# Optimization experiments

Measured on AMD Instinct MI355X. Metric: run time of the kernel, lower is better.

Reference implementation:

```python
import jax, jax.numpy as jnp
import numpy as np

B, H, W, C, NH, K = 4, 56, 56, 128, 4, 7


def setup_inputs() -> dict:
    key = jax.random.key(0)
    ks = jax.random.split(key, 6)
    x = jax.random.normal(ks[0], (B, H, W, C), dtype=jnp.float32)
    w_qkv = jax.random.normal(ks[1], (C, 3 * C), dtype=jnp.float32) * 0.02
    b_qkv = jnp.zeros((3 * C,), dtype=jnp.float32)
    rpb = jax.random.normal(ks[2], (NH, 2 * K - 1, 2 * K - 1), dtype=jnp.float32) * 0.02
    w_proj = jax.random.normal(ks[3], (C, C), dtype=jnp.float32) * 0.02
    b_proj = jnp.zeros((C,), dtype=jnp.float32)
    return {"x": x, "w_qkv": w_qkv, "b_qkv": b_qkv, "rpb": rpb,
            "w_proj": w_proj, "b_proj": b_proj}


def reference(x, w_qkv, b_qkv, rpb, w_proj, b_proj):
    B_, H_, W_, C_ = x.shape
    nh = rpb.shape[0]
    k = (rpb.shape[1] + 1) // 2          # kernel_size
    hd = C_ // nh                        # head_dim
    nb = k // 2                          # neighborhood radius
    scale = hd ** -0.5

    qkv = (x @ w_qkv + b_qkv).reshape(B_, H_, W_, 3, nh, hd)
    q = qkv[:, :, :, 0].transpose(0, 3, 1, 2, 4) * scale   # [B,nh,H,W,hd]
    kk = qkv[:, :, :, 1].transpose(0, 3, 1, 2, 4)          # [B,nh,H,W,hd]
    v = qkv[:, :, :, 2].transpose(0, 3, 1, 2, 4)           # [B,nh,H,W,hd]

    # NATTEN window start indices: window clamped to stay in-bounds (query shifts off-center at edges)
    si = jnp.clip(jnp.arange(H_) - nb, 0, H_ - k)          # [H]
    sj = jnp.clip(jnp.arange(W_) - nb, 0, W_ - k)          # [W]
    idx_i = si[:, None] + jnp.arange(k)                    # [H,k] absolute key rows
    idx_j = sj[:, None] + jnp.arange(k)                    # [W,k] absolute key cols

    # gather neighborhood keys/values: [B,nh,H,k,W,k,hd] (axes: b n i p j q d)
    k_win = kk[:, :, idx_i][:, :, :, :, idx_j]
    v_win = v[:, :, idx_i][:, :, :, :, idx_j]

    # relative position bias: index = key_pos - query_pos + (k-1)
    rel_i = idx_i - jnp.arange(H_)[:, None] + (k - 1)      # [H,k]
    rel_j = idx_j - jnp.arange(W_)[:, None] + (k - 1)      # [W,k]
    bias = rpb[:, rel_i][:, :, :, rel_j]                   # [nh,H,k,W,k]
    bias = bias.transpose(0, 1, 3, 2, 4)                   # [nh,H,W,k,k]

    attn = jnp.einsum('bnijd,bnipjqd->bnijpq', q, k_win) + bias[None]
    attn = jax.nn.softmax(attn.reshape(B_, nh, H_, W_, k * k), axis=-1)
    attn = attn.reshape(B_, nh, H_, W_, k, k)

    out = jnp.einsum('bnijpq,bnipjqd->bnijd', attn, v_win)  # [B,nh,H,W,hd]
    out = out.transpose(0, 2, 3, 1, 4).reshape(B_, H_, W_, C_)
    return out @ w_proj + b_proj
```

## Files before the change

kernel.cpp:

```cpp
#include <hip/hip_runtime.h>

#define BATCH 4
#define HH 56
#define WW 56
#define CC 128
#define NHD 4
#define HD 32
#define KS 7
#define NB 3
#define HWSZ (HH * WW)
#define RPBW 13
#define QKV_N 384
#define QKV_ELE ((size_t)BATCH * NHD * HWSZ * HD)

typedef unsigned short u16;
typedef unsigned int   u32;
typedef short bf16x8 __attribute__((ext_vector_type(8)));
typedef float f32x4  __attribute__((ext_vector_type(4)));

static __device__ __forceinline__ u32 f2bf(float f) {
    u32 u = __float_as_uint(f);
    return (u + 0x7FFFu + ((u >> 16) & 1u)) >> 16;
}
static __device__ __forceinline__ float bf2f(u32 h) { return __uint_as_float(h << 16); }

__global__ __launch_bounds__(256) void prep_w(
    const float* __restrict__ w_qkv, const float* __restrict__ w_proj,
    u16* __restrict__ wqT_h, u16* __restrict__ wqT_l,
    u16* __restrict__ wpT_h, u16* __restrict__ wpT_l)
{
    const int e = blockIdx.x * 256 + threadIdx.x;
    float v; u16 *dh, *dl; int idx;
    if (e < 384 * 128) {
        const int n = e >> 7, k = e & 127;
        v = w_qkv[k * QKV_N + n];
        dh = wqT_h; dl = wqT_l; idx = e;
    } else {
        const int e2 = e - 384 * 128;
        const int n = e2 >> 7, k = e2 & 127;
        v = w_proj[k * CC + n];
        dh = wpT_h; dl = wpT_l; idx = e2;
    }
    const u32 h = f2bf(v);
    dh[idx] = (u16)h;
    dl[idx] = (u16)f2bf(v - bf2f(h));
}

#define LP 72

__global__ __launch_bounds__(256) void qkv_mfma(
    const float* __restrict__ x, const u16* __restrict__ wT_h,
    const u16* __restrict__ wT_l, const float* __restrict__ bias,
    float* __restrict__ qb, float* __restrict__ kb, float* __restrict__ vb)
{
    __shared__ __align__(16) u16 Ah[64 * LP], Al[64 * LP];
    __shared__ __align__(16) u16 Bh[128 * LP], Bl[128 * LP];

    const int tid  = threadIdx.x;
    const int lane = tid & 63;
    const int w    = tid >> 6;
    const int wr = w >> 1, wc = w & 1;
    const int lr = lane >> 4, lc = lane & 15;
    const int m0 = blockIdx.x * 64;
    const int tz = blockIdx.y;

    f32x4 acc[2][4];
    #pragma unroll
    for (int nt = 0; nt < 4; ++nt) {
        const float bn = bias[tz * 128 + wc * 64 + nt * 16 + lc];
        acc[0][nt] = (f32x4){bn, bn, bn, bn};
        acc[1][nt] = acc[0][nt];
    }

    for (int kc = 0; kc < 128; kc += 64) {
        #pragma unroll
        for (int it = 0; it < 4; ++it) {
            const int task = tid + it * 256;
            const int row = task >> 4, q4 = task & 15;
            const float4 xv = *(const float4*)(x + (size_t)(m0 + row) * CC + kc + 4 * q4);
            const u32 h0 = f2bf(xv.x), h1 = f2bf(xv.y), h2 = f2bf(xv.z), h3 = f2bf(xv.w);
            const u32 l0 = f2bf(xv.x - bf2f(h0)), l1 = f2bf(xv.y - bf2f(h1));
            const u32 l2 = f2bf(xv.z - bf2f(h2)), l3 = f2bf(xv.w - bf2f(h3));
            const int off = row * LP + 4 * q4;
            *(uint2*)&Ah[off] = make_uint2(h0 | (h1 << 16), h2 | (h3 << 16));
            *(uint2*)&Al[off] = make_uint2(l0 | (l1 << 16), l2 | (l3 << 16));
        }
        #pragma unroll
        for (int it = 0; it < 8; ++it) {
            const int task = tid + it * 256;
            const int hl = task >> 10;
            const int t2 = task & 1023;
            const int n = t2 >> 3, q8 = t2 & 7;
            const u16* src = (hl ? wT_l : wT_h) + (size_t)(tz * 128 + n) * CC + kc + 8 * q8;
            const uint4 vv = *(const uint4*)src;
            u16* dst = (hl ? Bl : Bh) + n * LP + 8 * q8;
            *(uint4*)dst = vv;
        }
        __syncthreads();
        #pragma unroll
        for (int s = 0; s < 2; ++s) {
            const int ko = 32 * s + 8 * lr;
            bf16x8 bfh[4], bfl[4];
            #pragma unroll
            for (int nt = 0; nt < 4; ++nt) {
                const int bo = (wc * 64 + nt * 16 + lc) * LP + ko;
                bfh[nt] = *(const bf16x8*)&Bh[bo];
                bfl[nt] = *(const bf16x8*)&Bl[bo];
            }
            #pragma unroll
            for (int mt = 0; mt < 2; ++mt) {
                const int ao = (wr * 32 + mt * 16 + lc) * LP + ko;
                const bf16x8 afh = *(const bf16x8*)&Ah[ao];
                const bf16x8 afl = *(const bf16x8*)&Al[ao];
                #pragma unroll
                for (int nt = 0; nt < 4; ++nt) {
                    acc[mt][nt] = __builtin_amdgcn_mfma_f32_16x16x32_bf16(afh, bfh[nt], acc[mt][nt], 0, 0, 0);
                    acc[mt][nt] = __builtin_amdgcn_mfma_f32_16x16x32_bf16(afh, bfl[nt], acc[mt][nt], 0, 0, 0);
                    acc[mt][nt] = __builtin_amdgcn_mfma_f32_16x16x32_bf16(afl, bfh[nt], acc[mt][nt], 0, 0, 0);
                }
            }
        }
        __syncthreads();
    }

    float* dst      = (tz == 0) ? qb : (tz == 1) ? kb : vb;
    const float scl = (tz == 0) ? 0.17677669529663687f : 1.0f;
    const int b = m0 / HWSZ;
    #pragma unroll
    for (int mt = 0; mt < 2; ++mt) {
        #pragma unroll
        for (int nt = 0; nt < 4; ++nt) {
            const int n = wc * 64 + nt * 16 + lc;
            const int head = n >> 5, d = n & 31;
            #pragma unroll
            for (int r = 0; r < 4; ++r) {
                const int m  = m0 + wr * 32 + mt * 16 + lr * 4 + r;
                const int ij = m - b * HWSZ;
                dst[((size_t)(b * NHD + head) * HWSZ + ij) * HD + d] = acc[mt][nt][r] * scl;
            }
        }
    }
}

__global__ __launch_bounds__(256) void natten_attn(
    const float* __restrict__ qb, const float* __restrict__ kb,
    const float* __restrict__ vb, const float* __restrict__ rpb,
    float* __restrict__ ob)
{
    __shared__ float4 Ks[8][197];
    __shared__ float4 Vs[8][197];
    __shared__ float rpbs[RPBW * RPBW];

    const int tid = threadIdx.x;
    const int qid = tid >> 2;
    const int sub = tid & 3;
    const int qi_l = qid >> 3;
    const int qj_l = qid & 7;
    const int ti = blockIdx.x / 7;
    const int tj = blockIdx.x % 7;
    const int head = blockIdx.y;
    const int b    = blockIdx.z;
    const int qi = ti * 8 + qi_l;
    const int qj = tj * 8 + qj_l;
    const int R0 = min(max(ti * 8 - NB, 0), HH - 14);
    const int C0 = min(max(tj * 8 - NB, 0), WW - 14);

    const size_t base = (size_t)(b * NHD + head) * HWSZ;

    if (tid < RPBW * RPBW) rpbs[tid] = rpb[head * (RPBW * RPBW) + tid];

    for (int idx = tid; idx < 1568; idx += 256) {
        const int pos = idx >> 3;
        const int c   = idx & 7;
        const int ri  = pos / 14;
        const int rj  = pos - ri * 14;
        const size_t g = (base + (size_t)(R0 + ri) * WW + (C0 + rj)) * HD;
        Ks[c][pos] = ((const float4*)(kb + g))[c];
        Vs[c][pos] = ((const float4*)(vb + g))[c];
    }

    const int c0 = sub * 2;
    const float4* qp = (const float4*)(qb + (base + (size_t)qi * WW + qj) * HD) + c0;
    const float4 q0 = qp[0];
    const float4 q1 = qp[1];

    const int si  = min(max(qi - NB, 0), HH - KS);
    const int sj  = min(max(qj - NB, 0), WW - KS);
    const int ri0 = si - R0;
    const int rj0 = sj - C0;
    const int oi  = si - qi + (KS - 1);
    const int oj  = sj - qj + (KS - 1);

    __syncthreads();

    float s[49];
    #pragma unroll
    for (int pi = 0; pi < 7; ++pi) {
        const int rowoff = (ri0 + pi) * 14 + rj0;
        const int boff   = (oi + pi) * RPBW + oj;
        #pragma unroll
        for (int pj = 0; pj < 7; ++pj) {
            const int pos = rowoff + pj;
            const float4 k0 = Ks[c0][pos];
            const float4 k1 = Ks[c0 + 1][pos];
            float d = q0.x * k0.x + q0.y * k0.y + q0.z * k0.z + q0.w * k0.w
                    + q1.x * k1.x + q1.y * k1.y + q1.z * k1.z + q1.w * k1.w;
            d += __shfl_xor(d, 1, 64);
            d += __shfl_xor(d, 2, 64);
            s[pi * 7 + pj] = d + rpbs[boff + pj];
        }
    }

    float m = s[0];
    #pragma unroll
    for (int p = 1; p < 49; ++p) m = fmaxf(m, s[p]);
    float l = 0.f;
    #pragma unroll
    for (int p = 0; p < 49; ++p) { s[p] = __expf(s[p] - m); l += s[p]; }
    const float inv = 1.f / l;

    float4 o0 = make_float4(0.f, 0.f, 0.f, 0.f);
    float4 o1 = make_float4(0.f, 0.f, 0.f, 0.f);
    #pragma unroll
    for (int pi = 0; pi < 7; ++pi) {
        const int rowoff = (ri0 + pi) * 14 + rj0;
        #pragma unroll
        for (int pj = 0; pj < 7; ++pj) {
            const int pos = rowoff + pj;
            const float wt = s[pi * 7 + pj];
            const float4 v0 = Vs[c0][pos];
            const float4 v1 = Vs[c0 + 1][pos];
            o0.x += wt * v0.x; o0.y += wt * v0.y; o0.z += wt * v0.z; o0.w += wt * v0.w;
            o1.x += wt * v1.x; o1.y += wt * v1.y; o1.z += wt * v1.z; o1.w += wt * v1.w;
        }
    }

    float* op = ob + ((size_t)b * HWSZ + (size_t)qi * WW + qj) * CC + head * HD + sub * 8;
    ((float4*)op)[0] = make_float4(o0.x * inv, o0.y * inv, o0.z * inv, o0.w * inv);
    ((float4*)op)[1] = make_float4(o1.x * inv, o1.y * inv, o1.z * inv, o1.w * inv);
}

__global__ __launch_bounds__(256) void proj_mfma(
    const float* __restrict__ a, const u16* __restrict__ wT_h,
    const u16* __restrict__ wT_l, const float* __restrict__ bias,
    float* __restrict__ out)
{
    __shared__ __align__(16) u16 Ah[32 * LP], Al[32 * LP];
    __shared__ __align__(16) u16 Bh[128 * LP], Bl[128 * LP];

    const int tid  = threadIdx.x;
    const int lane = tid & 63;
    const int w    = tid >> 6;
    const int wr = w >> 1, wc = w & 1;
    const int lr = lane >> 4, lc = lane & 15;
    const int m0 = blockIdx.x * 32;

    f32x4 acc[4];
    #pragma unroll
    for (int nt = 0; nt < 4; ++nt) {
        const float bn = bias[wc * 64 + nt * 16 + lc];
        acc[nt] = (f32x4){bn, bn, bn, bn};
    }

    for (int kc = 0; kc < 128; kc += 64) {
        #pragma unroll
        for (int it = 0; it < 2; ++it) {
            const int task = tid + it * 256;
            const int row = task >> 4, q4 = task & 15;
            const float4 xv = *(const float4*)(a + (size_t)(m0 + row) * CC + kc + 4 * q4);
            const u32 h0 = f2bf(xv.x), h1 = f2bf(xv.y), h2 = f2bf(xv.z), h3 = f2bf(xv.w);
            const u32 l0 = f2bf(xv.x - bf2f(h0)), l1 = f2bf(xv.y - bf2f(h1));
            const u32 l2 = f2bf(xv.z - bf2f(h2)), l3 = f2bf(xv.w - bf2f(h3));
            const int off = row * LP + 4 * q4;
            *(uint2*)&Ah[off] = make_uint2(h0 | (h1 << 16), h2 | (h3 << 16));
            *(uint2*)&Al[off] = make_uint2(l0 | (l1 << 16), l2 | (l3 << 16));
        }
        #pragma unroll
        for (int it = 0; it < 8; ++it) {
            const int task = tid + it * 256;
            const int hl = task >> 10;
            const int t2 = task & 1023;
            const int n = t2 >> 3, q8 = t2 & 7;
            const u16* src = (hl ? wT_l : wT_h) + (size_t)n * CC + kc + 8 * q8;
            const uint4 vv = *(const uint4*)src;
            u16* dst = (hl ? Bl : Bh) + n * LP + 8 * q8;
            *(uint4*)dst = vv;
        }
        __syncthreads();
        #pragma unroll
        for (int s = 0; s < 2; ++s) {
            const int ko = 32 * s + 8 * lr;
            const int ao = (wr * 16 + lc) * LP + ko;
            const bf16x8 afh = *(const bf16x8*)&Ah[ao];
            const bf16x8 afl = *(const bf16x8*)&Al[ao];
            #pragma unroll
            for (int nt = 0; nt < 4; ++nt) {
                const int bo = (wc * 64 + nt * 16 + lc) * LP + ko;
                const bf16x8 bh = *(const bf16x8*)&Bh[bo];
                const bf16x8 bl = *(const bf16x8*)&Bl[bo];
                acc[nt] = __builtin_amdgcn_mfma_f32_16x16x32_bf16(afh, bh, acc[nt], 0, 0, 0);
                acc[nt] = __builtin_amdgcn_mfma_f32_16x16x32_bf16(afh, bl, acc[nt], 0, 0, 0);
                acc[nt] = __builtin_amdgcn_mfma_f32_16x16x32_bf16(afl, bh, acc[nt], 0, 0, 0);
            }
        }
        __syncthreads();
    }

    #pragma unroll
    for (int nt = 0; nt < 4; ++nt) {
        const int n = wc * 64 + nt * 16 + lc;
        #pragma unroll
        for (int r = 0; r < 4; ++r) {
            const int m = m0 + wr * 16 + lr * 4 + r;
            out[(size_t)m * CC + n] = acc[nt][r];
        }
    }
}

extern "C" void kernel_launch(void* const* d_in, const int* in_sizes, int n_in,
                              void* d_out, int out_size, void* d_ws, size_t ws_size,
                              hipStream_t stream) {
    const float* x      = (const float*)d_in[0];
    const float* w_qkv  = (const float*)d_in[1];
    const float* b_qkv  = (const float*)d_in[2];
    const float* rpb    = (const float*)d_in[3];
    const float* w_proj = (const float*)d_in[4];
    const float* b_proj = (const float*)d_in[5];
    float* out = (float*)d_out;

    float* ws  = (float*)d_ws;
    float* qbf = ws;
    float* kbf = ws + QKV_ELE;
    float* vbf = ws + 2 * QKV_ELE;
    float* obf = ws + 3 * QKV_ELE;
    u16* wqT_h = (u16*)(ws + 4 * QKV_ELE);
    u16* wqT_l = wqT_h + 384 * 128;
    u16* wpT_h = wqT_l + 384 * 128;
    u16* wpT_l = wpT_h + 128 * 128;

    prep_w<<<256, 256, 0, stream>>>(w_qkv, w_proj, wqT_h, wqT_l, wpT_h, wpT_l);
    qkv_mfma<<<dim3(196, 3), 256, 0, stream>>>(x, wqT_h, wqT_l, b_qkv, qbf, kbf, vbf);
    natten_attn<<<dim3(49, NHD, BATCH), 256, 0, stream>>>(qbf, kbf, vbf, rpb, obf);
    proj_mfma<<<392, 256, 0, stream>>>(obf, wpT_h, wpT_l, b_proj, out);
}
```

Baseline: 110.9 us.

## Move neighborhood attention QK and PV onto split-bf16 MFMA tiles

Rewrites the attention kernel so each wave computes scores for 16 queries against a contiguous band of 8x16 key positions with bf16 MFMA, using a hi/lo split to keep near-fp32 accuracy. It then masks positions outside the 7x7 window, does the softmax across lanes, and runs the PV product as MFMA over a transposed, padded V tile in LDS. Elsewhere the manual fp32-to-bf16 rounding is replaced by the packed v_cvt_pk_bf16_f32 instruction. This drops the scalar FMA and shuffle-reduction work, but it computes many masked, wasted scores per window, adds LDS conversion and layout cost, and changes rounding behaviour.

Result: no change. 108.8 us (-1.9%).

```diff
diff --git a/kernel.cpp b/kernel.cpp
--- a/kernel.cpp
+++ b/kernel.cpp
@@ -16,6 +16,7 @@
 typedef unsigned short u16;
 typedef unsigned int   u32;
 typedef short bf16x8 __attribute__((ext_vector_type(8)));
+typedef short bf16x4 __attribute__((ext_vector_type(4)));
 typedef float f32x4  __attribute__((ext_vector_type(4)));
 
 static __device__ __forceinline__ u32 f2bf(float f) {
@@ -23,6 +24,26 @@
     return (u + 0x7FFFu + ((u >> 16) & 1u)) >> 16;
 }
 static __device__ __forceinline__ float bf2f(u32 h) { return __uint_as_float(h << 16); }
+
+static __device__ __forceinline__ u32 cvtpk(float lo, float hi) {
+    u32 d;
+    asm("v_cvt_pk_bf16_f32 %0, %1, %2" : "=v"(d) : "v"(lo), "v"(hi));
+    return d;
+}
+static __device__ __forceinline__ void split2(float a, float b, u32& h, u32& l) {
+    h = cvtpk(a, b);
+    l = cvtpk(a - __uint_as_float(h << 16), b - __uint_as_float(h & 0xffff0000u));
+}
+
+#if __has_builtin(__builtin_amdgcn_mfma_f32_16x16x16bf16_1k)
+#define MFMA16(a, b, c) __builtin_amdgcn_mfma_f32_16x16x16bf16_1k(a, b, c, 0, 0, 0)
+#else
+static __device__ __forceinline__ f32x4 mfma16_asm(bf16x4 a, bf16x4 b, f32x4 c) {
+    asm("v_mfma_f32_16x16x16_bf16 %0, %1, %2, %0" : "+v"(c) : "v"(a), "v"(b));
+    return c;
+}
+#define MFMA16(a, b, c) mfma16_asm(a, b, c)
+#endif
 
 __global__ __launch_bounds__(256) void prep_w(
     const float* __restrict__ w_qkv, const float* __restrict__ w_proj,
@@ -78,12 +99,12 @@
             const int task = tid + it * 256;
             const int row = task >> 4, q4 = task & 15;
             const float4 xv = *(const float4*)(x + (size_t)(m0 + row) * CC + kc + 4 * q4);
-            const u32 h0 = f2bf(xv.x), h1 = f2bf(xv.y), h2 = f2bf(xv.z), h3 = f2bf(xv.w);
-            const u32 l0 = f2bf(xv.x - bf2f(h0)), l1 = f2bf(xv.y - bf2f(h1));
-            const u32 l2 = f2bf(xv.z - bf2f(h2)), l3 = f2bf(xv.w - bf2f(h3));
+            u32 h0, l0, h1, l1;
+            split2(xv.x, xv.y, h0, l0);
+            split2(xv.z, xv.w, h1, l1);
             const int off = row * LP + 4 * q4;
-            *(uint2*)&Ah[off] = make_uint2(h0 | (h1 << 16), h2 | (h3 << 16));
-            *(uint2*)&Al[off] = make_uint2(l0 | (l1 << 16), l2 | (l3 << 16));
+            *(uint2*)&Ah[off] = make_uint2(h0, h1);
+            *(uint2*)&Al[off] = make_uint2(l0, l1);
         }
         #pragma unroll
         for (int it = 0; it < 8; ++it) {
@@ -123,8 +144,9 @@
         __syncthreads();
     }
 
-    float* dst      = (tz == 0) ? qb : (tz == 1) ? kb : vb;
-    const float scl = (tz == 0) ? 0.17677669529663687f : 1.0f;
+    const int tzz = tz;
+    float* dst      = (tzz == 0) ? qb : (tzz == 1) ? kb : vb;
+    const float scl = (tzz == 0) ? 0.17677669529663687f : 1.0f;
     const int b = m0 / HWSZ;
     #pragma unroll
     for (int mt = 0; mt < 2; ++mt) {
@@ -147,97 +169,180 @@
     const float* __restrict__ vb, const float* __restrict__ rpb,
     float* __restrict__ ob)
 {
-    __shared__ float4 Ks[8][197];
-    __shared__ float4 Vs[8][197];
+    __shared__ __align__(16) u16 KhS[208 * 32];
+    __shared__ __align__(16) u16 KlS[208 * 32];
+    __shared__ __align__(16) u16 VhS[26 * 16 * 20];
+    __shared__ __align__(16) u16 VlS[26 * 16 * 20];
     __shared__ float rpbs[RPBW * RPBW];
 
-    const int tid = threadIdx.x;
-    const int qid = tid >> 2;
-    const int sub = tid & 3;
-    const int qi_l = qid >> 3;
-    const int qj_l = qid & 7;
+    const int tid  = threadIdx.x;
+    const int lane = tid & 63;
+    const int wv   = tid >> 6;
+    const int g    = lane >> 4;
+    const int cl   = lane & 15;
+
     const int ti = blockIdx.x / 7;
     const int tj = blockIdx.x % 7;
     const int head = blockIdx.y;
     const int b    = blockIdx.z;
-    const int qi = ti * 8 + qi_l;
-    const int qj = tj * 8 + qj_l;
     const int R0 = min(max(ti * 8 - NB, 0), HH - 14);
     const int C0 = min(max(tj * 8 - NB, 0), WW - 14);
-
     const size_t base = (size_t)(b * NHD + head) * HWSZ;
 
+    const int qlq = 16 * wv + cl;
+    const int qi  = ti * 8 + (qlq >> 3);
+    const int qj  = tj * 8 + (qlq & 7);
+    const float* qp = qb + (base + (size_t)qi * WW + qj) * HD + 8 * g;
+    const float4 qv0 = *(const float4*)qp;
+    const float4 qv1 = *(const float4*)(qp + 4);
+
+    union U8 { u32 u[4]; bf16x8 v; };
+    U8 uqh, uql;
+    split2(qv0.x, qv0.y, uqh.u[0], uql.u[0]);
+    split2(qv0.z, qv0.w, uqh.u[1], uql.u[1]);
+    split2(qv1.x, qv1.y, uqh.u[2], uql.u[2]);
+    split2(qv1.z, qv1.w, uqh.u[3], uql.u[3]);
+    const bf16x8 Qh = uqh.v;
+    const bf16x8 Ql = uql.v;
+
     if (tid < RPBW * RPBW) rpbs[tid] = rpb[head * (RPBW * RPBW) + tid];
 
     for (int idx = tid; idx < 1568; idx += 256) {
-        const int pos = idx >> 3;
-        const int c   = idx & 7;
-        const int ri  = pos / 14;
-        const int rj  = pos - ri * 14;
-        const size_t g = (base + (size_t)(R0 + ri) * WW + (C0 + rj)) * HD;
-        Ks[c][pos] = ((const float4*)(kb + g))[c];
-        Vs[c][pos] = ((const float4*)(vb + g))[c];
-    }
-
-    const int c0 = sub * 2;
-    const float4* qp = (const float4*)(qb + (base + (size_t)qi * WW + qj) * HD) + c0;
-    const float4 q0 = qp[0];
-    const float4 q1 = qp[1];
-
-    const int si  = min(max(qi - NB, 0), HH - KS);
-    const int sj  = min(max(qj - NB, 0), WW - KS);
-    const int ri0 = si - R0;
-    const int rj0 = sj - C0;
-    const int oi  = si - qi + (KS - 1);
-    const int oj  = sj - qj + (KS - 1);
-
+        const int pos = idx >> 3, c4 = idx & 7;
+        const int ri = (pos * 293) >> 12;
+        const int rj = pos - ri * 14;
+        const float4 kv = *(const float4*)(kb + (base + (size_t)(R0 + ri) * WW + (C0 + rj)) * HD + 4 * c4);
+        u32 h0, l0, h1, l1;
+        split2(kv.x, kv.y, h0, l0);
+        split2(kv.z, kv.w, h1, l1);
+        *(uint2*)&KhS[pos * 32 + 4 * c4] = make_uint2(h0, h1);
+        *(uint2*)&KlS[pos * 32 + 4 * c4] = make_uint2(l0, l1);
+    }
+    for (int idx = tid; idx < 784; idx += 256) {
+        const int pr = idx >> 3, c4 = idx & 7;
+        const int pos0 = 2 * pr;
+        const int ri0 = (pos0 * 293) >> 12;       const int rj0 = pos0 - ri0 * 14;
+        const int ri1 = ((pos0 + 1) * 293) >> 12; const int rj1 = pos0 + 1 - ri1 * 14;
+        const float4 va = *(const float4*)(vb + (base + (size_t)(R0 + ri0) * WW + (C0 + rj0)) * HD + 4 * c4);
+        const float4 vc = *(const float4*)(vb + (base + (size_t)(R0 + ri1) * WW + (C0 + rj1)) * HD + 4 * c4);
+        const int t = pos0 >> 4, kk = pos0 & 15;
+        const float a0[4] = {va.x, va.y, va.z, va.w};
+        const float a1[4] = {vc.x, vc.y, vc.z, vc.w};
+        #pragma unroll
+        for (int i = 0; i < 4; ++i) {
+            const int d = 4 * c4 + i;
+            const int nt = d >> 4, cd = d & 15;
+            u32 hh, ll;
+            split2(a0[i], a1[i], hh, ll);
+            const int off = ((nt * 13 + t) * 16 + cd) * 20 + kk;
+            *(u32*)&VhS[off] = hh;
+            *(u32*)&VlS[off] = ll;
+        }
+    }
+    for (int idx = tid; idx < 384; idx += 256) {
+        const int kp = idx % 6;
+        int r = idx / 6;
+        const int cd = r & 15; r >>= 4;
+        const int nt = r & 1;  const int arr = r >> 1;
+        u16* dst = arr ? VlS : VhS;
+        *(u32*)&dst[((nt * 13 + 12) * 16 + cd) * 20 + 4 + 2 * kp] = 0u;
+    }
     __syncthreads();
 
-    float s[49];
-    #pragma unroll
-    for (int pi = 0; pi < 7; ++pi) {
-        const int rowoff = (ri0 + pi) * 14 + rj0;
-        const int boff   = (oi + pi) * RPBW + oj;
-        #pragma unroll
-        for (int pj = 0; pj < 7; ++pj) {
-            const int pos = rowoff + pj;
-            const float4 k0 = Ks[c0][pos];
-            const float4 k1 = Ks[c0 + 1][pos];
-            float d = q0.x * k0.x + q0.y * k0.y + q0.z * k0.z + q0.w * k0.w
-                    + q1.x * k1.x + q1.y * k1.y + q1.z * k1.z + q1.w * k1.w;
-            d += __shfl_xor(d, 1, 64);
-            d += __shfl_xor(d, 2, 64);
-            s[pi * 7 + pj] = d + rpbs[boff + pj];
-        }
-    }
-
-    float m = s[0];
-    #pragma unroll
-    for (int p = 1; p < 49; ++p) m = fmaxf(m, s[p]);
-    float l = 0.f;
-    #pragma unroll
-    for (int p = 0; p < 49; ++p) { s[p] = __expf(s[p] - m); l += s[p]; }
-    const float inv = 1.f / l;
-
-    float4 o0 = make_float4(0.f, 0.f, 0.f, 0.f);
-    float4 o1 = make_float4(0.f, 0.f, 0.f, 0.f);
-    #pragma unroll
-    for (int pi = 0; pi < 7; ++pi) {
-        const int rowoff = (ri0 + pi) * 14 + rj0;
-        #pragma unroll
-        for (int pj = 0; pj < 7; ++pj) {
-            const int pos = rowoff + pj;
-            const float wt = s[pi * 7 + pj];
-            const float4 v0 = Vs[c0][pos];
-            const float4 v1 = Vs[c0 + 1][pos];
-            o0.x += wt * v0.x; o0.y += wt * v0.y; o0.z += wt * v0.z; o0.w += wt * v0.w;
-            o1.x += wt * v1.x; o1.y += wt * v1.y; o1.z += wt * v1.z; o1.w += wt * v1.w;
-        }
-    }
-
-    float* op = ob + ((size_t)b * HWSZ + (size_t)qi * WW + qj) * CC + head * HD + sub * 8;
-    ((float4*)op)[0] = make_float4(o0.x * inv, o0.y * inv, o0.z * inv, o0.w * inv);
-    ((float4*)op)[1] = make_float4(o1.x * inv, o1.y * inv, o1.z * inv, o1.w * inv);
+    const int qi0  = ti * 8 + 2 * wv;
+    const int s_lo = min(max(qi0 - NB, 0), HH - KS);
+    const int t0   = min(((s_lo - R0) * 14) >> 4, 5);
+
+    f32x4 p[8];
+    #pragma unroll
+    for (int tt = 0; tt < 8; ++tt) p[tt] = (f32x4){0.f, 0.f, 0.f, 0.f};
+    #pragma unroll
+    for (int tt = 0; tt < 8; ++tt) {
+        const int ro = (16 * (t0 + tt) + cl) * 32 + 8 * g;
+        const bf16x8 kh = *(const bf16x8*)&KhS[ro];
+        const bf16x8 kl = *(const bf16x8*)&KlS[ro];
+        p[tt] = __builtin_amdgcn_mfma_f32_16x16x32_bf16(kh, Qh, p[tt], 0, 0, 0);
+        p[tt] = __builtin_amdgcn_mfma_f32_16x16x32_bf16(kh, Ql, p[tt], 0, 0, 0);
+        p[tt] = __builtin_amdgcn_mfma_f32_16x16x32_bf16(kl, Qh, p[tt], 0, 0, 0);
+    }
+
+    const int si = min(max(qi - NB, 0), HH - KS);
+    const int sj = min(max(qj - NB, 0), WW - KS);
+    const int r_si = si - R0, c_sj = sj - C0;
+    const int aq = qi - R0, bq = qj - C0;
+
+    float mmax = -3.0e38f;
+    #pragma unroll
+    for (int tt = 0; tt < 8; ++tt) {
+        #pragma unroll
+        for (int r = 0; r < 4; ++r) {
+            const int pp = 16 * (t0 + tt) + 4 * g + r;
+            const int rowp = (pp * 293) >> 12;
+            const int colp = pp - rowp * 14;
+            const bool ok = (pp < 196) && ((u32)(rowp - r_si) <= 6u) && ((u32)(colp - c_sj) <= 6u);
+            int bidx = (rowp - aq + 6) * RPBW + (colp - bq + 6);
+            bidx = ok ? bidx : 0;
+            const float sv = ok ? (p[tt][r] + rpbs[bidx]) : -3.0e38f;
+            p[tt][r] = sv;
+            mmax = fmaxf(mmax, sv);
+        }
+    }
+    mmax = fmaxf(mmax, __shfl_xor(mmax, 16, 64));
+    mmax = fmaxf(mmax, __shfl_xor(mmax, 32, 64));
+
+    float lsum = 0.f;
+    #pragma unroll
+    for (int tt = 0; tt < 8; ++tt) {
+        #pragma unroll
+        for (int r = 0; r < 4; ++r) {
+            const float e = __expf(p[tt][r] - mmax);
+            p[tt][r] = e;
+            lsum += e;
+        }
+    }
+    lsum += __shfl_xor(lsum, 16, 64);
+    lsum += __shfl_xor(lsum, 32, 64);
+    const float inv = 1.f / lsum;
+
+    bf16x4 pah[8], pal[8];
+    #pragma unroll
+    for (int tt = 0; tt < 8; ++tt) {
+        const float p0 = p[tt][0] * inv, p1 = p[tt][1] * inv;
+        const float p2 = p[tt][2] * inv, p3 = p[tt][3] * inv;
+        union U4 { u32 u[2]; bf16x4 v; } ua, ub;
+        split2(p0, p1, ua.u[0], ub.u[0]);
+        split2(p2, p3, ua.u[1], ub.u[1]);
+        pah[tt] = ua.v;
+        pal[tt] = ub.v;
+    }
+
+    f32x4 o[2];
+    o[0] = (f32x4){0.f, 0.f, 0.f, 0.f};
+    o[1] = (f32x4){0.f, 0.f, 0.f, 0.f};
+    #pragma unroll
+    for (int tt = 0; tt < 8; ++tt) {
+        const int t = t0 + tt;
+        #pragma unroll
+        for (int nt = 0; nt < 2; ++nt) {
+            const int off = ((nt * 13 + t) * 16 + cl) * 20 + 4 * g;
+            const bf16x4 vh = *(const bf16x4*)&VhS[off];
+            const bf16x4 vl = *(const bf16x4*)&VlS[off];
+            o[nt] = MFMA16(pah[tt], vh, o[nt]);
+            o[nt] = MFMA16(pal[tt], vh, o[nt]);
+            o[nt] = MFMA16(pah[tt], vl, o[nt]);
+        }
+    }
+
+    #pragma unroll
+    for (int nt = 0; nt < 2; ++nt) {
+        #pragma unroll
+        for (int r = 0; r < 4; ++r) {
+            const int qlo = 16 * wv + 4 * g + r;
+            const int oqi = ti * 8 + (qlo >> 3);
+            const int oqj = tj * 8 + (qlo & 7);
+            ob[((size_t)b * HWSZ + (size_t)oqi * WW + oqj) * CC + head * HD + 16 * nt + cl] = o[nt][r];
+        }
+    }
 }
 
 __global__ __launch_bounds__(256) void proj_mfma(
@@ -268,12 +373,12 @@
             const int task = tid + it * 256;
             const int row = task >> 4, q4 = task & 15;
             const float4 xv = *(const float4*)(a + (size_t)(m0 + row) * CC + kc + 4 * q4);
-            const u32 h0 = f2bf(xv.x), h1 = f2bf(xv.y), h2 = f2bf(xv.z), h3 = f2bf(xv.w);
-            const u32 l0 = f2bf(xv.x - bf2f(h0)), l1 = f2bf(xv.y - bf2f(h1));
-            const u32 l2 = f2bf(xv.z - bf2f(h2)), l3 = f2bf(xv.w - bf2f(h3));
+            u32 h0, l0, h1, l1;
+            split2(xv.x, xv.y, h0, l0);
+            split2(xv.z, xv.w, h1, l1);
             const int off = row * LP + 4 * q4;
-            *(uint2*)&Ah[off] = make_uint2(h0 | (h1 << 16), h2 | (h3 << 16));
-            *(uint2*)&Al[off] = make_uint2(l0 | (l1 << 16), l2 | (l3 << 16));
+            *(uint2*)&Ah[off] = make_uint2(h0, h1);
+            *(uint2*)&Al[off] = make_uint2(l0, l1);
         }
         #pragma unroll
         for (int it = 0; it < 8; ++it) {
```
